# Kernel optimization log

Hardware: AMD Instinct MI355X
Metric: run time of the kernel (lower is better)

## Reference

```python
import jax, jax.numpy as jnp
import numpy as np

K_SECTIONS = 8


def _make_sos(K=K_SECTIONS, seed=0):
    """Build K stable biquad sections [K, 6] = [b0,b1,b2,a0,a1,a2], unit DC gain."""
    rng = np.random.default_rng(seed)
    r_p = rng.uniform(0.5, 0.95, K)
    th_p = rng.uniform(0.1, 3.0, K)
    r_z = rng.uniform(0.5, 0.99, K)
    th_z = rng.uniform(0.1, 3.0, K)
    a1 = -2.0 * r_p * np.cos(th_p)
    a2 = r_p ** 2
    b1 = -2.0 * r_z * np.cos(th_z)
    b2 = r_z ** 2
    b0 = np.ones(K)
    g = (1.0 + a1 + a2) / (b0 + b1 + b2)  # normalize DC gain to 1 per section
    sos = np.stack([b0 * g, b1 * g, b2 * g, np.ones(K), a1, a2], axis=1)
    return jnp.asarray(sos, dtype=jnp.float32)


def setup_inputs() -> dict:
    key = jax.random.key(0)
    x = jax.random.normal(key, (128, 65536), dtype=jnp.float32)  # [C, T]
    return {"x": x, "sos": _make_sos()}


def reference(x, sos):
    """Fused SOS cascade: sequential direct-form-I biquad recurrence over time."""
    K = sos.shape[0]
    a0 = sos[:, 3]
    b0, b1, b2 = sos[:, 0] / a0, sos[:, 1] / a0, sos[:, 2] / a0  # [K]
    a1, a2 = sos[:, 4] / a0, sos[:, 5] / a0                      # [K]
    C, T = x.shape

    def step(carry, xt):  # xt: [C]
        x1, x2, y1, y2 = carry  # each [K, C]
        s = xt
        nx1, nx2, ny1, ny2 = [], [], [], []
        for k in range(K):  # fixed small unroll over cascaded sections
            y = (b0[k] * s + b1[k] * x1[k] + b2[k] * x2[k]
                 - a1[k] * y1[k] - a2[k] * y2[k])
            nx2.append(x1[k]); nx1.append(s)
            ny2.append(y1[k]); ny1.append(y)
            s = y
        carry = (jnp.stack(nx1), jnp.stack(nx2), jnp.stack(ny1), jnp.stack(ny2))
        return carry, s

    init = tuple(jnp.zeros((K, C), x.dtype) for _ in range(4))
    _, y = jax.lax.scan(step, init, x.T)  # scan over time axis -> y: [T, C]
    return y.T
```

## Files before the change

kernel.cpp:

```cpp
#include <hip/hip_runtime.h>


#define T_LEN   65536
#define CG      16
#define TB      1024
#define NTAP    144
#define HALO    128
#define XSPAN   (HALO + TB + 32)
#define XSTRIDE 1192
#define NQ4     (CG * (XSPAN / 4))
#define Q4ROW   (XSPAN / 4)
#define TPB     512
#define NSTAGE  (TPB - 64)

typedef _Float16 half8  __attribute__((ext_vector_type(8)));
typedef _Float16 half4h __attribute__((ext_vector_type(4)));
typedef float    f32x4  __attribute__((ext_vector_type(4)));

__global__ __launch_bounds__(TPB)
void FusedSOSCascade_20040317403806_kernel(const float* __restrict__ x,
                                           const float* __restrict__ sos,
                                           float* __restrict__ out) {
  __shared__ alignas(16) _Float16 lds_x[CG * XSTRIDE];
  __shared__ alignas(16) float hs[NTAP];

  const int tid = threadIdx.x;
  const int cg  = blockIdx.x & 7;
  const int tb  = blockIdx.x >> 3;
  const int c0  = cg * CG;
  const int t0  = tb * TB;

  if (tid < 64) {
    const int k = tid & 7;
    const float a0  = sos[k * 6 + 3];
    const float cb0 =  sos[k * 6 + 0] / a0;
    const float cb1 =  sos[k * 6 + 1] / a0;
    const float cb2 =  sos[k * 6 + 2] / a0;
    const float cn1 = -(sos[k * 6 + 4] / a0);
    const float cn2 = -(sos[k * 6 + 5] / a0);
    float y = 0.f, z1 = 0.f, z2 = 0.f;
#pragma unroll 4
    for (int n = 0; n < NTAP + 7; ++n) {
      const int ui = __builtin_amdgcn_update_dpp(0, __float_as_int(y),
                                                 0x111, 0xf, 0xf, true);
      float s = __int_as_float(ui);
      if (tid == 0) s = (n == 0) ? 1.f : 0.f;
      y  = fmaf(cb0, s, z1);
      z1 = fmaf(cb1, s, fmaf(cn1, y, z2));
      z2 = fmaf(cb2, s, cn2 * y);
      if (tid == 7 && n >= 7) hs[n - 7] = y;
    }
  } else {
    const int st = tid - 64;
#pragma unroll 1
    for (int k0 = 0; k0 < 11; k0 += 6) {
      float4 v[6];
      const int kn = (k0 == 0) ? 6 : 5;
#pragma unroll
      for (int j = 0; j < 6; ++j) {
        if (j < kn) {
          const int idx = st + (k0 + j) * NSTAGE;
          float4 t = make_float4(0.f, 0.f, 0.f, 0.f);
          if (idx < NQ4) {
            const int row = idx / Q4ROW;
            const int c4  = idx - row * Q4ROW;
            const int gt  = t0 - HALO + 4 * c4;
            if (gt >= 0 && gt < T_LEN)
              t = *(const float4*)(x + (size_t)(c0 + row) * T_LEN + gt);
          }
          v[j] = t;
        }
      }
#pragma unroll
      for (int j = 0; j < 6; ++j) {
        if (j < kn) {
          const int idx = st + (k0 + j) * NSTAGE;
          if (idx < NQ4) {
            const int row = idx / Q4ROW;
            const int c4  = idx - row * Q4ROW;
            half4h hv = { (_Float16)v[j].x, (_Float16)v[j].y,
                          (_Float16)v[j].z, (_Float16)v[j].w };
            *(half4h*)(&lds_x[row * XSTRIDE + 4 * c4]) = hv;
          }
        }
      }
    }
  }
  __syncthreads();

  const int wv = tid >> 6;
  const int l  = tid & 63;
  const int r  = l & 15;
  const int g  = l >> 4;

  half8 afrag[5];
#pragma unroll
  for (int m = 0; m < 5; ++m) {
    half8 af;
#pragma unroll
    for (int e = 0; e < 8; ++e) {
      const int i = r + 128 - 32 * m - 8 * g - e;
      const float hv = (i >= 0 && i < NTAP) ? hs[i] : 0.f;
      af[e] = (_Float16)hv;
    }
    afrag[m] = af;
  }

  float* orow = out + (size_t)(c0 + r) * T_LEN + t0;
#pragma unroll 1
  for (int q = 0; q < 8; ++q) {
    const int tt = wv * 8 + q;
    f32x4 acc = {0.f, 0.f, 0.f, 0.f};
#pragma unroll
    for (int m = 0; m < 5; ++m) {
      const half8 bfrag =
          *(const half8*)(&lds_x[r * XSTRIDE + 16 * tt + 32 * m + 8 * g]);
      acc = __builtin_amdgcn_mfma_f32_16x16x32_f16(afrag[m], bfrag, acc,
                                                   0, 0, 0);
    }
    *(float4*)(orow + 16 * tt + 4 * g) =
        make_float4(acc[0], acc[1], acc[2], acc[3]);
  }
}

extern "C" void kernel_launch(void* const* d_in, const int* in_sizes, int n_in,
                              void* d_out, int out_size, void* d_ws, size_t ws_size,
                              hipStream_t stream) {
  const float* x   = (const float*)d_in[0];
  const float* sos = (const float*)d_in[1];
  float* out = (float*)d_out;
  (void)in_sizes; (void)n_in; (void)out_size; (void)d_ws; (void)ws_size;

  FusedSOSCascade_20040317403806_kernel<<<dim3(512), dim3(TPB), 0, stream>>>(
      x, sos, out);
}
```

Baseline: 87.47 us.

## Precompute A-fragments in LDS table and reuse sliding X-fragments across MFMA steps

The first wave now builds the FIR-tap A-fragments once into a shared LDS table, and all waves load them from there. This replaces each thread's 40 scalar hs lookups with conversions. The MFMA loop now processes two output tiles (even and odd) at once, with two independent accumulator chains. It reuses overlapping X-fragments by shifting a 5-entry register window, so each step loads only one new fragment per chain. This cuts LDS reads and exposes more MFMA parallelism, at the cost of extra LDS, more registers and a fully unrolled loop.

```diff
diff --git a/kernel.cpp b/kernel.cpp
--- a/kernel.cpp
+++ b/kernel.cpp
@@ -23,6 +23,7 @@
                                            float* __restrict__ out) {
   __shared__ alignas(16) _Float16 lds_x[CG * XSTRIDE];
   __shared__ alignas(16) float hs[NTAP];
+  __shared__ alignas(16) _Float16 atab[64 * 5 * 8];
 
   const int tid = threadIdx.x;
   const int cg  = blockIdx.x & 7;
@@ -32,23 +33,40 @@
 
   if (tid < 64) {
     const int k = tid & 7;
-    const float a0  = sos[k * 6 + 3];
-    const float cb0 =  sos[k * 6 + 0] / a0;
-    const float cb1 =  sos[k * 6 + 1] / a0;
-    const float cb2 =  sos[k * 6 + 2] / a0;
-    const float cn1 = -(sos[k * 6 + 4] / a0);
-    const float cn2 = -(sos[k * 6 + 5] / a0);
-    float y = 0.f, z1 = 0.f, z2 = 0.f;
+    {
+      const float a0  = sos[k * 6 + 3];
+      const float cb0 =  sos[k * 6 + 0] / a0;
+      const float cb1 =  sos[k * 6 + 1] / a0;
+      const float cb2 =  sos[k * 6 + 2] / a0;
+      const float cn1 = -(sos[k * 6 + 4] / a0);
+      const float cn2 = -(sos[k * 6 + 5] / a0);
+      float y = 0.f, z1 = 0.f, z2 = 0.f;
 #pragma unroll 4
-    for (int n = 0; n < NTAP + 7; ++n) {
-      const int ui = __builtin_amdgcn_update_dpp(0, __float_as_int(y),
-                                                 0x111, 0xf, 0xf, true);
-      float s = __int_as_float(ui);
-      if (tid == 0) s = (n == 0) ? 1.f : 0.f;
-      y  = fmaf(cb0, s, z1);
-      z1 = fmaf(cb1, s, fmaf(cn1, y, z2));
-      z2 = fmaf(cb2, s, cn2 * y);
-      if (tid == 7 && n >= 7) hs[n - 7] = y;
+      for (int n = 0; n < NTAP + 7; ++n) {
+        const int ui = __builtin_amdgcn_update_dpp(0, __float_as_int(y),
+                                                   0x111, 0xf, 0xf, true);
+        float s = __int_as_float(ui);
+        if (tid == 0) s = (n == 0) ? 1.f : 0.f;
+        y  = fmaf(cb0, s, z1);
+        z1 = fmaf(cb1, s, fmaf(cn1, y, z2));
+        z2 = fmaf(cb2, s, cn2 * y);
+        if (tid == 7 && n >= 7) hs[n - 7] = y;
+      }
+    }
+    asm volatile("s_waitcnt lgkmcnt(0)" ::: "memory");
+    {
+      const int r = tid & 15, g = tid >> 4;
+#pragma unroll
+      for (int m = 0; m < 5; ++m) {
+        half8 af;
+#pragma unroll
+        for (int e = 0; e < 8; ++e) {
+          const int i = r + 128 - 32 * m - 8 * g - e;
+          const float hv = (i >= 0 && i < NTAP) ? hs[i] : 0.f;
+          af[e] = (_Float16)hv;
+        }
+        *(half8*)(&atab[(tid * 5 + m) * 8]) = af;
+      }
     }
   } else {
     const int st = tid - 64;
@@ -95,32 +113,45 @@
 
   half8 afrag[5];
 #pragma unroll
-  for (int m = 0; m < 5; ++m) {
-    half8 af;
+  for (int m = 0; m < 5; ++m)
+    afrag[m] = *(const half8*)(&atab[(l * 5 + m) * 8]);
+
+#define XFRAG(tt, m) \
+  (*(const half8*)(&lds_x[r * XSTRIDE + 16 * (tt) + 32 * (m) + 8 * g]))
+
+  const int te = wv * 8;
+  float* orow = out + (size_t)(c0 + r) * T_LEN + t0;
+
+  half8 E[5], O[5];
 #pragma unroll
-    for (int e = 0; e < 8; ++e) {
-      const int i = r + 128 - 32 * m - 8 * g - e;
-      const float hv = (i >= 0 && i < NTAP) ? hs[i] : 0.f;
-      af[e] = (_Float16)hv;
-    }
-    afrag[m] = af;
-  }
+  for (int m = 0; m < 5; ++m) E[m] = XFRAG(te, m);
+#pragma unroll
+  for (int m = 0; m < 5; ++m) O[m] = XFRAG(te + 1, m);
 
-  float* orow = out + (size_t)(c0 + r) * T_LEN + t0;
-#pragma unroll 1
-  for (int q = 0; q < 8; ++q) {
-    const int tt = wv * 8 + q;
-    f32x4 acc = {0.f, 0.f, 0.f, 0.f};
+#pragma unroll
+  for (int q = 0; q < 4; ++q) {
+    f32x4 accE = {0.f, 0.f, 0.f, 0.f};
+    f32x4 accO = {0.f, 0.f, 0.f, 0.f};
 #pragma unroll
     for (int m = 0; m < 5; ++m) {
-      const half8 bfrag =
-          *(const half8*)(&lds_x[r * XSTRIDE + 16 * tt + 32 * m + 8 * g]);
-      acc = __builtin_amdgcn_mfma_f32_16x16x32_f16(afrag[m], bfrag, acc,
-                                                   0, 0, 0);
+      accE = __builtin_amdgcn_mfma_f32_16x16x32_f16(afrag[m], E[m], accE,
+                                                    0, 0, 0);
+      accO = __builtin_amdgcn_mfma_f32_16x16x32_f16(afrag[m], O[m], accO,
+                                                    0, 0, 0);
     }
-    *(float4*)(orow + 16 * tt + 4 * g) =
-        make_float4(acc[0], acc[1], acc[2], acc[3]);
+    const int ttE = te + 2 * q;
+    *(float4*)(orow + 16 * ttE + 4 * g) =
+        make_float4(accE[0], accE[1], accE[2], accE[3]);
+    *(float4*)(orow + 16 * (ttE + 1) + 4 * g) =
+        make_float4(accO[0], accO[1], accO[2], accO[3]);
+    if (q < 3) {
+#pragma unroll
+      for (int m = 0; m < 4; ++m) { E[m] = E[m + 1]; O[m] = O[m + 1]; }
+      E[4] = XFRAG(ttE + 2, 4);
+      O[4] = XFRAG(ttE + 3, 4);
+    }
   }
+#undef XFRAG
 }
 
 extern "C" void kernel_launch(void* const* d_in, const int* in_sizes, int n_in,
```

Result: no change. 87.44 us (-0.0%).

## Split input staging in two phases and overlap second load with MFMA compute

Applied to the files above, without the earlier changes.

The input tile load is split: the first part (halo plus first half of the block) is staged before the barrier, and the second part is loaded into registers and then issued while the first half of outputs is computed with MFMA, stored to LDS afterward, followed by a second barrier. The A-fragment (impulse response Toeplitz) is precomputed once into an LDS table by the filter wave instead of every thread gathering it from hs. The MFMA loop is restructured to process two output tiles at once, reusing sliding B fragments across consecutive tiles. This aims to hide global load latency and reduce LDS reads, at the cost of an extra barrier and more register pressure.

```diff
diff --git a/kernel.cpp b/kernel.cpp
--- a/kernel.cpp
+++ b/kernel.cpp
@@ -8,9 +8,11 @@
 #define HALO    128
 #define XSPAN   (HALO + TB + 32)
 #define XSTRIDE 1192
-#define NQ4     (CG * (XSPAN / 4))
-#define Q4ROW   (XSPAN / 4)
 #define TPB     512
+#define AQ      166
+#define BQ      130
+#define NA4     (CG * AQ)
+#define NB4     (CG * BQ)
 #define NSTAGE  (TPB - 64)
 
 typedef _Float16 half8  __attribute__((ext_vector_type(8)));
@@ -22,7 +24,8 @@
                                            const float* __restrict__ sos,
                                            float* __restrict__ out) {
   __shared__ alignas(16) _Float16 lds_x[CG * XSTRIDE];
-  __shared__ alignas(16) float hs[NTAP];
+  __shared__ float hs[NTAP];
+  __shared__ alignas(16) _Float16 atab[64 * 5 * 8];
 
   const int tid = threadIdx.x;
   const int cg  = blockIdx.x & 7;
@@ -32,61 +35,84 @@
 
   if (tid < 64) {
     const int k = tid & 7;
-    const float a0  = sos[k * 6 + 3];
-    const float cb0 =  sos[k * 6 + 0] / a0;
-    const float cb1 =  sos[k * 6 + 1] / a0;
-    const float cb2 =  sos[k * 6 + 2] / a0;
-    const float cn1 = -(sos[k * 6 + 4] / a0);
-    const float cn2 = -(sos[k * 6 + 5] / a0);
-    float y = 0.f, z1 = 0.f, z2 = 0.f;
+    {
+      const float a0  = sos[k * 6 + 3];
+      const float cb0 =  sos[k * 6 + 0] / a0;
+      const float cb1 =  sos[k * 6 + 1] / a0;
+      const float cb2 =  sos[k * 6 + 2] / a0;
+      const float cn1 = -(sos[k * 6 + 4] / a0);
+      const float cn2 = -(sos[k * 6 + 5] / a0);
+      float y = 0.f, z1 = 0.f, z2 = 0.f;
 #pragma unroll 4
-    for (int n = 0; n < NTAP + 7; ++n) {
-      const int ui = __builtin_amdgcn_update_dpp(0, __float_as_int(y),
-                                                 0x111, 0xf, 0xf, true);
-      float s = __int_as_float(ui);
-      if (tid == 0) s = (n == 0) ? 1.f : 0.f;
-      y  = fmaf(cb0, s, z1);
-      z1 = fmaf(cb1, s, fmaf(cn1, y, z2));
-      z2 = fmaf(cb2, s, cn2 * y);
-      if (tid == 7 && n >= 7) hs[n - 7] = y;
+      for (int n = 0; n < NTAP + 7; ++n) {
+        const int ui = __builtin_amdgcn_update_dpp(0, __float_as_int(y),
+                                                   0x111, 0xf, 0xf, true);
+        float s = __int_as_float(ui);
+        if (tid == 0) s = (n == 0) ? 1.f : 0.f;
+        y  = fmaf(cb0, s, z1);
+        z1 = fmaf(cb1, s, fmaf(cn1, y, z2));
+        z2 = fmaf(cb2, s, cn2 * y);
+        if (tid == 7 && n >= 7) hs[n - 7] = y;
+      }
+    }
+    asm volatile("s_waitcnt lgkmcnt(0)" ::: "memory");
+    {
+      const int rr = tid & 15, gg = tid >> 4;
+#pragma unroll
+      for (int m = 0; m < 5; ++m) {
+        half8 af;
+#pragma unroll
+        for (int e = 0; e < 8; ++e) {
+          const int i = rr + 128 - 32 * m - 8 * gg - e;
+          af[e] = (_Float16)((i >= 0 && i < NTAP) ? hs[i] : 0.f);
+        }
+        *(half8*)(&atab[(tid * 5 + m) * 8]) = af;
+      }
     }
   } else {
     const int st = tid - 64;
-#pragma unroll 1
-    for (int k0 = 0; k0 < 11; k0 += 6) {
-      float4 v[6];
-      const int kn = (k0 == 0) ? 6 : 5;
+    float4 v[6];
 #pragma unroll
-      for (int j = 0; j < 6; ++j) {
-        if (j < kn) {
-          const int idx = st + (k0 + j) * NSTAGE;
-          float4 t = make_float4(0.f, 0.f, 0.f, 0.f);
-          if (idx < NQ4) {
-            const int row = idx / Q4ROW;
-            const int c4  = idx - row * Q4ROW;
-            const int gt  = t0 - HALO + 4 * c4;
-            if (gt >= 0 && gt < T_LEN)
-              t = *(const float4*)(x + (size_t)(c0 + row) * T_LEN + gt);
-          }
-          v[j] = t;
-        }
+    for (int k = 0; k < 6; ++k) {
+      const int idx = st + k * NSTAGE;
+      float4 t = make_float4(0.f, 0.f, 0.f, 0.f);
+      if (idx < NA4) {
+        const int row = idx / AQ;
+        const int c4  = idx - row * AQ;
+        const int gt  = t0 - HALO + 4 * c4;
+        if (gt >= 0 && gt < T_LEN)
+          t = *(const float4*)(x + (size_t)(c0 + row) * T_LEN + gt);
       }
+      v[k] = t;
+    }
 #pragma unroll
-      for (int j = 0; j < 6; ++j) {
-        if (j < kn) {
-          const int idx = st + (k0 + j) * NSTAGE;
-          if (idx < NQ4) {
-            const int row = idx / Q4ROW;
-            const int c4  = idx - row * Q4ROW;
-            half4h hv = { (_Float16)v[j].x, (_Float16)v[j].y,
-                          (_Float16)v[j].z, (_Float16)v[j].w };
-            *(half4h*)(&lds_x[row * XSTRIDE + 4 * c4]) = hv;
-          }
-        }
+    for (int k = 0; k < 6; ++k) {
+      const int idx = st + k * NSTAGE;
+      if (idx < NA4) {
+        const int row = idx / AQ;
+        const int c4  = idx - row * AQ;
+        half4h hv = { (_Float16)v[k].x, (_Float16)v[k].y,
+                      (_Float16)v[k].z, (_Float16)v[k].w };
+        *(half4h*)(&lds_x[row * XSTRIDE + 4 * c4]) = hv;
       }
     }
   }
   __syncthreads();
+
+  float4 vb[5];
+#pragma unroll
+  for (int k = 0; k < 5; ++k) {
+    const int idx = tid + k * TPB;
+    float4 t = make_float4(0.f, 0.f, 0.f, 0.f);
+    if (idx < NB4) {
+      const int row = idx / BQ;
+      const int j   = idx - row * BQ;
+      const int gt  = t0 - HALO + 4 * (AQ + j);
+      if (gt < T_LEN)
+        t = *(const float4*)(x + (size_t)(c0 + row) * T_LEN + gt);
+    }
+    vb[k] = t;
+  }
 
   const int wv = tid >> 6;
   const int l  = tid & 63;
@@ -95,32 +121,67 @@
 
   half8 afrag[5];
 #pragma unroll
-  for (int m = 0; m < 5; ++m) {
-    half8 af;
-#pragma unroll
-    for (int e = 0; e < 8; ++e) {
-      const int i = r + 128 - 32 * m - 8 * g - e;
-      const float hv = (i >= 0 && i < NTAP) ? hs[i] : 0.f;
-      af[e] = (_Float16)hv;
-    }
-    afrag[m] = af;
-  }
+  for (int m = 0; m < 5; ++m)
+    afrag[m] = *(const half8*)(&atab[(l * 5 + m) * 8]);
+
+#define XFRAG(tt, m) \
+  (*(const half8*)(&lds_x[r * XSTRIDE + 16 * (tt) + 32 * (m) + 8 * g]))
 
   float* orow = out + (size_t)(c0 + r) * T_LEN + t0;
-#pragma unroll 1
-  for (int q = 0; q < 8; ++q) {
-    const int tt = wv * 8 + q;
-    f32x4 acc = {0.f, 0.f, 0.f, 0.f};
+
+#define COMPUTE_HALF(TT0)                                                    \
+  do {                                                                       \
+    const int tt0 = (TT0);                                                   \
+    half8 E[5], O[5];                                                        \
+    _Pragma("unroll")                                                        \
+    for (int m = 0; m < 5; ++m) E[m] = XFRAG(tt0, m);                        \
+    _Pragma("unroll")                                                        \
+    for (int m = 0; m < 5; ++m) O[m] = XFRAG(tt0 + 1, m);                    \
+    _Pragma("unroll")                                                        \
+    for (int q = 0; q < 2; ++q) {                                            \
+      half8 nE, nO;                                                          \
+      if (q == 0) { nE = XFRAG(tt0 + 2, 4); nO = XFRAG(tt0 + 3, 4); }        \
+      f32x4 accE = {0.f, 0.f, 0.f, 0.f};                                     \
+      f32x4 accO = {0.f, 0.f, 0.f, 0.f};                                     \
+      _Pragma("unroll")                                                      \
+      for (int m = 0; m < 5; ++m) {                                          \
+        accE = __builtin_amdgcn_mfma_f32_16x16x32_f16(afrag[m], E[m], accE,  \
+                                                      0, 0, 0);              \
+        accO = __builtin_amdgcn_mfma_f32_16x16x32_f16(afrag[m], O[m], accO,  \
+                                                      0, 0, 0);              \
+      }                                                                      \
+      const int ttE = tt0 + 2 * q;                                           \
+      *(float4*)(orow + 16 * ttE + 4 * g) =                                  \
+          make_float4(accE[0], accE[1], accE[2], accE[3]);                   \
+      *(float4*)(orow + 16 * (ttE + 1) + 4 * g) =                            \
+          make_float4(accO[0], accO[1], accO[2], accO[3]);                   \
+      if (q == 0) {                                                          \
+        _Pragma("unroll")                                                    \
+        for (int m = 0; m < 4; ++m) { E[m] = E[m + 1]; O[m] = O[m + 1]; }    \
+        E[4] = nE; O[4] = nO;                                                \
+      }                                                                      \
+    }                                                                        \
+  } while (0)
+
+  COMPUTE_HALF(wv * 4);
+
 #pragma unroll
-    for (int m = 0; m < 5; ++m) {
-      const half8 bfrag =
-          *(const half8*)(&lds_x[r * XSTRIDE + 16 * tt + 32 * m + 8 * g]);
-      acc = __builtin_amdgcn_mfma_f32_16x16x32_f16(afrag[m], bfrag, acc,
-                                                   0, 0, 0);
+  for (int k = 0; k < 5; ++k) {
+    const int idx = tid + k * TPB;
+    if (idx < NB4) {
+      const int row = idx / BQ;
+      const int j   = idx - row * BQ;
+      half4h hv = { (_Float16)vb[k].x, (_Float16)vb[k].y,
+                    (_Float16)vb[k].z, (_Float16)vb[k].w };
+      *(half4h*)(&lds_x[row * XSTRIDE + 4 * (AQ + j)]) = hv;
     }
-    *(float4*)(orow + 16 * tt + 4 * g) =
-        make_float4(acc[0], acc[1], acc[2], acc[3]);
   }
+  __syncthreads();
+
+  COMPUTE_HALF(32 + wv * 4);
+
+#undef COMPUTE_HALF
+#undef XFRAG
 }
 
 extern "C" void kernel_launch(void* const* d_in, const int* in_sizes, int n_in,
```

Result: no change. 87.99 us (+0.6%).

## Assign one channel per wavefront, drop block barrier, overlap loads with impulse computation

Applied to the files above, without the earlier changes.

Work is re-split so each 64-lane wave owns one channel over a 2048-sample span. It stages that channel's own halo-extended fp16 window in LDS and computes its own copy of the 144-tap impulse response, so the block-wide __syncthreads is replaced by a per-wave lgkmcnt wait. Global loads are issued into registers before the serial DPP impulse-response recurrence, so memory latency overlaps that serial chain. The MFMA tiling is remapped so the 16 columns are time sub-blocks of one channel rather than 16 channels. The halo overhead per output also shrinks. The cost is that every wave redundantly runs the 151-step serial impulse computation, and the blocks are smaller, with twice as many of them.

```diff
diff --git a/kernel.cpp b/kernel.cpp
--- a/kernel.cpp
+++ b/kernel.cpp
@@ -1,17 +1,13 @@
 #include <hip/hip_runtime.h>
 
 
-#define T_LEN   65536
-#define CG      16
-#define TB      1024
-#define NTAP    144
-#define HALO    128
-#define XSPAN   (HALO + TB + 32)
-#define XSTRIDE 1192
-#define NQ4     (CG * (XSPAN / 4))
-#define Q4ROW   (XSPAN / 4)
-#define TPB     512
-#define NSTAGE  (TPB - 64)
+#define T_LEN  65536
+#define NTAP   144
+#define NCHB   4
+#define TSPAN  2048
+#define XROW   (128 + TSPAN + 32)
+#define NF4    (XROW / 4)
+#define TPB    (NCHB * 64)
 
 typedef _Float16 half8  __attribute__((ext_vector_type(8)));
 typedef _Float16 half4h __attribute__((ext_vector_type(4)));
@@ -21,17 +17,32 @@
 void FusedSOSCascade_20040317403806_kernel(const float* __restrict__ x,
                                            const float* __restrict__ sos,
                                            float* __restrict__ out) {
-  __shared__ alignas(16) _Float16 lds_x[CG * XSTRIDE];
-  __shared__ alignas(16) float hs[NTAP];
+  __shared__ alignas(16) _Float16 lds_x[NCHB][XROW];
+  __shared__ float hs[NCHB][NTAP];
 
   const int tid = threadIdx.x;
-  const int cg  = blockIdx.x & 7;
-  const int tb  = blockIdx.x >> 3;
-  const int c0  = cg * CG;
-  const int t0  = tb * TB;
+  const int wv  = tid >> 6;
+  const int l   = tid & 63;
+  const int cgi = blockIdx.x & 31;
+  const int tb  = blockIdx.x >> 5;
+  const int ch  = cgi * NCHB + wv;
+  const int t0  = tb * TSPAN;
+  const float* xr = x + (size_t)ch * T_LEN;
 
-  if (tid < 64) {
-    const int k = tid & 7;
+  float4 v[9];
+#pragma unroll
+  for (int it = 0; it < 9; ++it) {
+    const int idx = l + (it << 6);
+    float4 t = make_float4(0.f, 0.f, 0.f, 0.f);
+    if (idx < NF4) {
+      const int gt = t0 - 128 + (idx << 2);
+      if (gt >= 0 && gt < T_LEN) t = *(const float4*)(xr + gt);
+    }
+    v[it] = t;
+  }
+
+  {
+    const int k = l & 7;
     const float a0  = sos[k * 6 + 3];
     const float cb0 =  sos[k * 6 + 0] / a0;
     const float cb1 =  sos[k * 6 + 1] / a0;
@@ -44,55 +55,27 @@
       const int ui = __builtin_amdgcn_update_dpp(0, __float_as_int(y),
                                                  0x111, 0xf, 0xf, true);
       float s = __int_as_float(ui);
-      if (tid == 0) s = (n == 0) ? 1.f : 0.f;
+      if (l == 0) s = (n == 0) ? 1.f : 0.f;
       y  = fmaf(cb0, s, z1);
       z1 = fmaf(cb1, s, fmaf(cn1, y, z2));
       z2 = fmaf(cb2, s, cn2 * y);
-      if (tid == 7 && n >= 7) hs[n - 7] = y;
-    }
-  } else {
-    const int st = tid - 64;
-#pragma unroll 1
-    for (int k0 = 0; k0 < 11; k0 += 6) {
-      float4 v[6];
-      const int kn = (k0 == 0) ? 6 : 5;
-#pragma unroll
-      for (int j = 0; j < 6; ++j) {
-        if (j < kn) {
-          const int idx = st + (k0 + j) * NSTAGE;
-          float4 t = make_float4(0.f, 0.f, 0.f, 0.f);
-          if (idx < NQ4) {
-            const int row = idx / Q4ROW;
-            const int c4  = idx - row * Q4ROW;
-            const int gt  = t0 - HALO + 4 * c4;
-            if (gt >= 0 && gt < T_LEN)
-              t = *(const float4*)(x + (size_t)(c0 + row) * T_LEN + gt);
-          }
-          v[j] = t;
-        }
-      }
-#pragma unroll
-      for (int j = 0; j < 6; ++j) {
-        if (j < kn) {
-          const int idx = st + (k0 + j) * NSTAGE;
-          if (idx < NQ4) {
-            const int row = idx / Q4ROW;
-            const int c4  = idx - row * Q4ROW;
-            half4h hv = { (_Float16)v[j].x, (_Float16)v[j].y,
-                          (_Float16)v[j].z, (_Float16)v[j].w };
-            *(half4h*)(&lds_x[row * XSTRIDE + 4 * c4]) = hv;
-          }
-        }
-      }
+      if (l == 7 && n >= 7) hs[wv][n - 7] = y;
     }
   }
-  __syncthreads();
 
-  const int wv = tid >> 6;
-  const int l  = tid & 63;
-  const int r  = l & 15;
-  const int g  = l >> 4;
+#pragma unroll
+  for (int it = 0; it < 9; ++it) {
+    const int idx = l + (it << 6);
+    if (idx < NF4) {
+      half4h hv = { (_Float16)v[it].x, (_Float16)v[it].y,
+                    (_Float16)v[it].z, (_Float16)v[it].w };
+      *(half4h*)(&lds_x[wv][idx << 2]) = hv;
+    }
+  }
+  asm volatile("s_waitcnt lgkmcnt(0)" ::: "memory");
 
+  const int r = l & 15;
+  const int g = l >> 4;
   half8 afrag[5];
 #pragma unroll
   for (int m = 0; m < 5; ++m) {
@@ -100,25 +83,22 @@
 #pragma unroll
     for (int e = 0; e < 8; ++e) {
       const int i = r + 128 - 32 * m - 8 * g - e;
-      const float hv = (i >= 0 && i < NTAP) ? hs[i] : 0.f;
-      af[e] = (_Float16)hv;
+      af[e] = (_Float16)((i >= 0 && i < NTAP) ? hs[wv][i] : 0.f);
     }
     afrag[m] = af;
   }
 
-  float* orow = out + (size_t)(c0 + r) * T_LEN + t0;
-#pragma unroll 1
-  for (int q = 0; q < 8; ++q) {
-    const int tt = wv * 8 + q;
+  float* orow = out + (size_t)ch * T_LEN + t0;
+#pragma unroll
+  for (int t = 0; t < 8; ++t) {
+    const _Float16* bp = &lds_x[wv][(t << 8) + 16 * r + 8 * g];
     f32x4 acc = {0.f, 0.f, 0.f, 0.f};
 #pragma unroll
     for (int m = 0; m < 5; ++m) {
-      const half8 bfrag =
-          *(const half8*)(&lds_x[r * XSTRIDE + 16 * tt + 32 * m + 8 * g]);
-      acc = __builtin_amdgcn_mfma_f32_16x16x32_f16(afrag[m], bfrag, acc,
-                                                   0, 0, 0);
+      acc = __builtin_amdgcn_mfma_f32_16x16x32_f16(
+                afrag[m], *(const half8*)(bp + 32 * m), acc, 0, 0, 0);
     }
-    *(float4*)(orow + 16 * tt + 4 * g) =
+    *(float4*)(orow + (t << 8) + 16 * r + 4 * g) =
         make_float4(acc[0], acc[1], acc[2], acc[3]);
   }
 }
@@ -131,6 +111,6 @@
   float* out = (float*)d_out;
   (void)in_sizes; (void)n_in; (void)out_size; (void)d_ws; (void)ws_size;
 
-  FusedSOSCascade_20040317403806_kernel<<<dim3(512), dim3(TPB), 0, stream>>>(
+  FusedSOSCascade_20040317403806_kernel<<<dim3(1024), dim3(TPB), 0, stream>>>(
       x, sos, out);
 }
```

Measured after the change: 90.01 us. 2.9% more time.
